# Performance work log

Hardware: AMD Instinct MI355X
Metric: run time of the kernel (lower is better)

The kernel has to match this reference:

```python
import jax, jax.numpy as jnp
import numpy as np

NUM_EXPERTS = 8
TOP_K = 2
N_EMBD = 1024
BLOCK_SIZE = 128
# d_ffn = round_up(4*n_embd // top_k, block_size)
D_FFN = ((4 * N_EMBD // TOP_K + BLOCK_SIZE - 1) // BLOCK_SIZE) * BLOCK_SIZE  # 2048
TOTAL_WIDTH = NUM_EXPERTS * D_FFN  # 16384


def setup_inputs() -> dict:
    key = jax.random.key(0)
    k1, k2, k3, k4 = jax.random.split(key, 4)
    x = jax.random.normal(k1, (4, 2048, N_EMBD), dtype=jnp.float32)
    # router: nn.Linear(n_embd, num_experts, bias=False) -> weight [E, n_embd]
    w_router = jax.random.normal(k2, (NUM_EXPERTS, N_EMBD), dtype=jnp.float32) * 0.02
    w1 = jax.random.normal(k3, (N_EMBD, TOTAL_WIDTH), dtype=jnp.float32) * 0.02
    w2 = jax.random.normal(k4, (TOTAL_WIDTH, N_EMBD), dtype=jnp.float32) * 0.02
    return {"x": x, "w_router": w_router, "w1": w1, "w2": w2}


def reference(x, w_router, w1, w2):
    B, S, N = x.shape
    T = B * S
    x_flat = x.reshape(T, N)

    # Router
    router_logits = x_flat @ w_router.T                       # [T, E]
    router_probs = jax.nn.softmax(router_logits.astype(jnp.float32), axis=-1)
    expert_weights, selected_experts = jax.lax.top_k(router_probs, TOP_K)  # [T, K]
    # norm_topk_prob=True
    expert_weights = expert_weights / expert_weights.sum(axis=-1, keepdims=True)
    expert_weights = expert_weights.astype(x.dtype)

    # Expert computation. The original does a sort/gather + block-sparse grouped
    # GEMM; math-equivalently, each token's output is
    #   sum_k w_k * gelu(x @ W1_e) @ W2_e  for e = selected_experts[:, k].
    # Loop over the small fixed expert set, masking per-token combine weights.
    out = jnp.zeros((T, N), dtype=x.dtype)
    for e in range(NUM_EXPERTS):
        off = e * D_FFN
        # combine weight for expert e per token (0 if not routed there)
        w_e = jnp.where(selected_experts == e, expert_weights, 0.0).sum(axis=-1)  # [T]
        h = jax.nn.gelu(x_flat @ w1[:, off:off + D_FFN], approximate=False)       # [T, D_FFN]
        out = out + w_e[:, None] * (h @ w2[off:off + D_FFN, :])

    output = out.reshape(B, S, N)

    # Aux losses
    router_z_loss = jnp.mean(jax.nn.logsumexp(router_logits, axis=-1) ** 2)
    p_i = router_probs.mean(axis=0).astype(x.dtype)            # [E]
    flat_sel = selected_experts.reshape(-1)
    f_i = jnp.zeros((NUM_EXPERTS,), dtype=x.dtype).at[flat_sel].add(1.0 / flat_sel.shape[0])
    load_balance_loss = NUM_EXPERTS * (f_i @ p_i)

    return output, router_z_loss, load_balance_loss, f_i
```

## Files before the change

### kernel.cpp

```cpp
#include <hip/hip_runtime.h>
#include <hip/hip_bf16.h>
#include <math.h>

#define T_TOK 8192
#define NE 1024
#define N_EXP 8
#define DFFN 2048
#define TW 16384
#define P_TOT 16384

#define BMT 128
#define BNT 128
#define BK9 32

typedef __attribute__((ext_vector_type(8))) short bf16x8;
typedef __attribute__((ext_vector_type(4))) float f32x4;

#define GLOAD_LDS16(g, l) __builtin_amdgcn_global_load_lds( \
    (const __attribute__((address_space(1))) void*)(g), \
    (__attribute__((address_space(3))) void*)(l), 16, 0, 0)

static __device__ __forceinline__ unsigned short f2bf(float f) {
    __hip_bfloat16 b = __float2bfloat16(f);
    return *(unsigned short*)&b;
}

static __device__ __forceinline__ float gelu_fast(float v) {
    float u2 = v * (1.5957691216f + 0.0713548162f * v * v);
    return v / (1.f + __expf(-u2));
}

__global__ __launch_bounds__(256) void router_kernel(
    const float* __restrict__ x, const float* __restrict__ wr,
    int* __restrict__ sel_idx, float* __restrict__ sel_wt,
    float* __restrict__ z_part, float* __restrict__ p_part,
    unsigned short* __restrict__ xb)
{
    __shared__ float wrs[N_EXP * NE];
    __shared__ float zred[32];
    __shared__ float pred[32][8];
    int tid = threadIdx.x;
    for (int i = tid; i < N_EXP * NE / 4; i += 256)
        ((float4*)wrs)[i] = ((const float4*)wr)[i];
    __syncthreads();

    int slot = tid >> 3, oct = tid & 7;
    int t = blockIdx.x * 32 + slot;
    float lg[N_EXP];
#pragma unroll
    for (int e = 0; e < N_EXP; e++) lg[e] = 0.f;

    const float4* x4 = (const float4*)(x + (size_t)t * NE) + oct * 32;
    for (int n4 = 0; n4 < 32; n4++) {
        float4 xv = x4[n4];
        ushort4 o;
        o.x = f2bf(xv.x); o.y = f2bf(xv.y); o.z = f2bf(xv.z); o.w = f2bf(xv.w);
        *(ushort4*)&xb[(size_t)t * NE + oct * 128 + n4 * 4] = o;
#pragma unroll
        for (int e = 0; e < N_EXP; e++) {
            const float* w = &wrs[e * NE + oct * 128 + n4 * 4];
            lg[e] += xv.x * w[0] + xv.y * w[1] + xv.z * w[2] + xv.w * w[3];
        }
    }
#pragma unroll
    for (int d = 1; d < 8; d <<= 1)
#pragma unroll
        for (int e = 0; e < N_EXP; e++) lg[e] += __shfl_xor(lg[e], d);

    float m = lg[0];
#pragma unroll
    for (int e = 1; e < N_EXP; e++) m = fmaxf(m, lg[e]);
    float p[N_EXP], s = 0.f;
#pragma unroll
    for (int e = 0; e < N_EXP; e++) { p[e] = expf(lg[e] - m); s += p[e]; }
    float inv = 1.f / s;
#pragma unroll
    for (int e = 0; e < N_EXP; e++) p[e] *= inv;
    float lse = m + logf(s);

    int e0 = 0;
#pragma unroll
    for (int e = 1; e < N_EXP; e++) if (p[e] > p[e0]) e0 = e;
    int e1 = (e0 == 0) ? 1 : 0;
#pragma unroll
    for (int e = 0; e < N_EXP; e++) if (e != e0 && p[e] > p[e1]) e1 = e;

    if (oct == 0) {
        float wn = 1.f / (p[e0] + p[e1]);
        sel_idx[t * 2 + 0] = e0;
        sel_idx[t * 2 + 1] = e1;
        sel_wt[t * 2 + 0] = p[e0] * wn;
        sel_wt[t * 2 + 1] = p[e1] * wn;
        zred[slot] = lse * lse;
#pragma unroll
        for (int e = 0; e < N_EXP; e++) pred[slot][e] = p[e];
    }
    __syncthreads();
    if (tid == 0) {
        float zs = 0.f;
        for (int i = 0; i < 32; i++) zs += zred[i];
        z_part[blockIdx.x] = zs;
        for (int e = 0; e < N_EXP; e++) {
            float ps = 0.f;
            for (int i = 0; i < 32; i++) ps += pred[i][e];
            p_part[blockIdx.x * N_EXP + e] = ps;
        }
    }
}

__global__ __launch_bounds__(256) void finalize_router(
    const int* __restrict__ sel_idx,
    const float* __restrict__ z_part, const float* __restrict__ p_part,
    int* __restrict__ cnt, int* __restrict__ off, int* __restrict__ cursor,
    int* __restrict__ tile_tab, int* __restrict__ tile_n,
    float* __restrict__ out)
{
    __shared__ int redc[256];
    __shared__ int cnts[N_EXP];
    int tid = threadIdx.x;
    int c[N_EXP];
#pragma unroll
    for (int e = 0; e < N_EXP; e++) c[e] = 0;
    for (int i = tid; i < P_TOT; i += 256) c[sel_idx[i]]++;
#pragma unroll
    for (int e = 0; e < N_EXP; e++) {
        redc[tid] = c[e];
        __syncthreads();
        for (int st = 128; st > 0; st >>= 1) {
            if (tid < st) redc[tid] += redc[tid + st];
            __syncthreads();
        }
        if (tid == 0) cnts[e] = redc[0];
        __syncthreads();
    }
    if (tid == 0) {
        int o = 0;
        int nt = 0;
        for (int e = 0; e < N_EXP; e++) {
            cnt[e] = cnts[e];
            off[e] = o;
            o += cnts[e];
            cursor[e] = 0;
            for (int rb = 0; rb < cnts[e]; rb += BMT)
                tile_tab[nt++] = (e << 20) | rb;
        }
        off[N_EXP] = o;
        tile_n[0] = nt;
        float zs = 0.f;
        for (int b = 0; b < 256; b++) zs += z_part[b];
        float lb = 0.f;
        float* tail = out + (size_t)T_TOK * NE;
        for (int e = 0; e < N_EXP; e++) {
            float ps = 0.f;
            for (int b = 0; b < 256; b++) ps += p_part[b * N_EXP + e];
            float fi = (float)cnts[e] / (float)P_TOT;
            float pi = ps / (float)T_TOK;
            lb += fi * pi;
            tail[2 + e] = fi;
        }
        tail[0] = zs / (float)T_TOK;
        tail[1] = 8.f * lb;
    }
}

__global__ __launch_bounds__(256) void scatter_kernel(
    const int* __restrict__ sel_idx, const int* __restrict__ off,
    int* __restrict__ cursor, int* __restrict__ token_list)
{
    int i = blockIdx.x * 256 + threadIdx.x;
    if (i < P_TOT) {
        int e = sel_idx[i];
        int pos = atomicAdd(&cursor[e], 1);
        token_list[off[e] + pos] = i;
    }
}

__global__ __launch_bounds__(256) void transpose_bf16_kernel(
    const float* __restrict__ src, unsigned short* __restrict__ dst,
    int R, int C)
{
    __shared__ float tile[64][65];
    int rb = blockIdx.y * 64, cb = blockIdx.x * 64;
    int tid = threadIdx.x;
#pragma unroll
    for (int p = 0; p < 4; p++) {
        int idx = p * 256 + tid;
        int r = idx >> 4, c4 = (idx & 15) << 2;
        float4 v = *(const float4*)&src[(size_t)(rb + r) * C + cb + c4];
        tile[r][c4 + 0] = v.x; tile[r][c4 + 1] = v.y;
        tile[r][c4 + 2] = v.z; tile[r][c4 + 3] = v.w;
    }
    __syncthreads();
#pragma unroll
    for (int p = 0; p < 4; p++) {
        int idx = p * 256 + tid;
        int c = idx >> 4, r4 = (idx & 15) << 2;
        ushort4 o;
        o.x = f2bf(tile[r4 + 0][c]); o.y = f2bf(tile[r4 + 1][c]);
        o.z = f2bf(tile[r4 + 2][c]); o.w = f2bf(tile[r4 + 3][c]);
        *(ushort4*)&dst[(size_t)(cb + c) * R + rb + r4] = o;
    }
}

#define STG(buf, kb) do {                                                 \
    GLOAD_LDS16(asrc0 + (kb), &As[buf][wid * 1024]);                      \
    GLOAD_LDS16(asrc1 + (kb), &As[buf][wid * 1024 + 512]);                \
    GLOAD_LDS16(bsrc0 + (kb), &Bs[buf][wid * 1024]);                      \
    GLOAD_LDS16(bsrc1 + (kb), &Bs[buf][wid * 1024 + 512]);                \
} while (0)

#define GEMM_LOOP(NKT)                                                    \
    STG(0, 0);                                                            \
    for (int t = 0; t < (NKT); t++) {                                     \
        int cur = t & 1;                                                  \
        if (t + 1 < (NKT)) {                                              \
            STG(cur ^ 1, (t + 1) * BK9);                                  \
            asm volatile("s_waitcnt vmcnt(4)" ::: "memory");              \
        } else {                                                          \
            asm volatile("s_waitcnt vmcnt(0)" ::: "memory");              \
        }                                                                 \
        __builtin_amdgcn_s_barrier();                                     \
        __builtin_amdgcn_sched_barrier(0);                                \
        bf16x8 af[4], bfr[4];                                             \
        _Pragma("unroll")                                                 \
        for (int m = 0; m < 4; m++)                                       \
            af[m] = *(const bf16x8*)&As[cur][(wm * 64 + m * 16 + rr) * BK9 + kqa * 8]; \
        _Pragma("unroll")                                                 \
        for (int n = 0; n < 4; n++)                                       \
            bfr[n] = *(const bf16x8*)&Bs[cur][(wn * 64 + n * 16 + rr) * BK9 + kqa * 8]; \
        __builtin_amdgcn_s_setprio(1);                                    \
        _Pragma("unroll")                                                 \
        for (int m = 0; m < 4; m++)                                       \
            _Pragma("unroll")                                             \
            for (int n = 0; n < 4; n++)                                   \
                acc[m][n] = __builtin_amdgcn_mfma_f32_16x16x32_bf16(      \
                    af[m], bfr[n], acc[m][n], 0, 0, 0);                   \
        __builtin_amdgcn_s_setprio(0);                                    \
        __builtin_amdgcn_sched_barrier(0);                                \
        __builtin_amdgcn_s_barrier();                                     \
    }

__global__ __launch_bounds__(256, 4) void gemm1_mfma(
    const __hip_bfloat16* __restrict__ xb, const __hip_bfloat16* __restrict__ w1t,
    const int* __restrict__ token_list, const float* __restrict__ sel_wt,
    const int* __restrict__ cnt, const int* __restrict__ off,
    const int* __restrict__ tile_tab, const int* __restrict__ tile_n,
    __hip_bfloat16* __restrict__ h)
{
    __shared__ __align__(16) __hip_bfloat16 As[2][BMT * BK9];
    __shared__ __align__(16) __hip_bfloat16 Bs[2][BNT * BK9];

    int b = blockIdx.x;
    int slot = b & 7, idx = b >> 3;
    int rowt = idx >> 1;
    if (rowt >= tile_n[0]) return;
    int colbase = (slot * 2 + (idx & 1)) * BNT;
    int tab = tile_tab[rowt];
    int e = tab >> 20, rowbase = tab & 0xFFFFF;
    int off_e = off[e];
    int rows_e = cnt[e] - rowbase;

    int tid = threadIdx.x;
    int wid = tid >> 6, lane = tid & 63;
    int wm = wid >> 1, wn = wid & 1;
    int rr = lane & 15, kq = lane >> 4;
    int kqa = kq ^ ((rr >> 1) & 3);
    int ksw = (lane & 3) ^ ((lane >> 3) & 3);

    int r0 = wid * 32 + (lane >> 2);
    int r1 = r0 + 16;
    int ent0 = token_list[off_e + rowbase + ((r0 < rows_e) ? r0 : 0)];
    int ent1 = token_list[off_e + rowbase + ((r1 < rows_e) ? r1 : 0)];
    const __hip_bfloat16* asrc0 = xb + (size_t)(ent0 >> 1) * NE + ksw * 8;
    const __hip_bfloat16* asrc1 = xb + (size_t)(ent1 >> 1) * NE + ksw * 8;
    const __hip_bfloat16* bsrc0 = w1t + (size_t)(e * DFFN + colbase + r0) * NE + ksw * 8;
    const __hip_bfloat16* bsrc1 = bsrc0 + (size_t)16 * NE;

    f32x4 acc[4][4] = {};
    GEMM_LOOP(NE / BK9)

    int colg = colbase + wn * 64;
#pragma unroll
    for (int m = 0; m < 4; m++) {
#pragma unroll
        for (int j = 0; j < 4; j++) {
            int r = wm * 64 + m * 16 + kq * 4 + j;
            if (r < rows_e) {
                size_t p = (size_t)off_e + rowbase + r;
                float wgt = sel_wt[token_list[p]];
#pragma unroll
                for (int n = 0; n < 4; n++) {
                    float g = gelu_fast(acc[m][n][j]);
                    h[p * DFFN + colg + n * 16 + rr] = __float2bfloat16(wgt * g);
                }
            }
        }
    }
}

__global__ __launch_bounds__(256, 4) void gemm2_mfma(
    const __hip_bfloat16* __restrict__ h, const __hip_bfloat16* __restrict__ w2t,
    const int* __restrict__ token_list,
    const int* __restrict__ cnt, const int* __restrict__ off,
    const int* __restrict__ tile_tab, const int* __restrict__ tile_n,
    float* __restrict__ out)
{
    __shared__ __align__(16) __hip_bfloat16 As[2][BMT * BK9];
    __shared__ __align__(16) __hip_bfloat16 Bs[2][BNT * BK9];

    int b = blockIdx.x;
    int slot = b & 7, rowt = b >> 3;
    if (rowt >= tile_n[0]) return;
    int colbase = slot * BNT;
    int tab = tile_tab[rowt];
    int e = tab >> 20, rowbase = tab & 0xFFFFF;
    int off_e = off[e];
    int rows_e = cnt[e] - rowbase;

    int tid = threadIdx.x;
    int wid = tid >> 6, lane = tid & 63;
    int wm = wid >> 1, wn = wid & 1;
    int rr = lane & 15, kq = lane >> 4;
    int kqa = kq ^ ((rr >> 1) & 3);
    int ksw = (lane & 3) ^ ((lane >> 3) & 3);

    int r0 = wid * 32 + (lane >> 2);
    int r1 = r0 + 16;
    int pr0 = off_e + rowbase + ((r0 < rows_e) ? r0 : 0);
    int pr1 = off_e + rowbase + ((r1 < rows_e) ? r1 : 0);
    const __hip_bfloat16* asrc0 = h + (size_t)pr0 * DFFN + ksw * 8;
    const __hip_bfloat16* asrc1 = h + (size_t)pr1 * DFFN + ksw * 8;
    const __hip_bfloat16* bsrc0 = w2t + (size_t)(colbase + r0) * TW + e * DFFN + ksw * 8;
    const __hip_bfloat16* bsrc1 = bsrc0 + (size_t)16 * TW;

    f32x4 acc[4][4] = {};
    GEMM_LOOP(DFFN / BK9)

    int colg = colbase + wn * 64;
#pragma unroll
    for (int m = 0; m < 4; m++) {
#pragma unroll
        for (int j = 0; j < 4; j++) {
            int r = wm * 64 + m * 16 + kq * 4 + j;
            if (r < rows_e) {
                size_t p = (size_t)off_e + rowbase + r;
                int tok = token_list[p] >> 1;
#pragma unroll
                for (int n = 0; n < 4; n++)
                    atomicAdd(&out[(size_t)tok * NE + colg + n * 16 + rr],
                              acc[m][n][j]);
            }
        }
    }
}

extern "C" void kernel_launch(void* const* d_in, const int* in_sizes, int n_in,
                              void* d_out, int out_size, void* d_ws, size_t ws_size,
                              hipStream_t stream)
{
    const float* x  = (const float*)d_in[0];
    const float* wr = (const float*)d_in[1];
    const float* w1 = (const float*)d_in[2];
    const float* w2 = (const float*)d_in[3];
    float* out = (float*)d_out;

    char* ws = (char*)d_ws;
    size_t o = 0;
    __hip_bfloat16* h   = (__hip_bfloat16*)(ws + o); o += (size_t)P_TOT * DFFN * 2;
    __hip_bfloat16* xb  = (__hip_bfloat16*)(ws + o); o += (size_t)T_TOK * NE * 2;
    __hip_bfloat16* w1t = (__hip_bfloat16*)(ws + o); o += (size_t)NE * TW * 2;
    __hip_bfloat16* w2t = (__hip_bfloat16*)(ws + o); o += (size_t)TW * NE * 2;
    int*   sel_idx    = (int*)(ws + o);   o += P_TOT * 4;
    float* sel_wt     = (float*)(ws + o); o += P_TOT * 4;
    int*   token_list = (int*)(ws + o);   o += P_TOT * 4;
    int*   cnt        = (int*)(ws + o);   o += 64;
    int*   off        = (int*)(ws + o);   o += 64;
    int*   cursor     = (int*)(ws + o);   o += 64;
    int*   tile_tab   = (int*)(ws + o);   o += 256 * 4;
    int*   tile_n     = (int*)(ws + o);   o += 64;
    float* z_part     = (float*)(ws + o); o += 256 * 4;
    float* p_part     = (float*)(ws + o); o += 256 * N_EXP * 4;

    hipMemsetAsync(d_out, 0, (size_t)out_size * sizeof(float), stream);

    router_kernel<<<256, 256, 0, stream>>>(x, wr, sel_idx, sel_wt, z_part, p_part,
                                           (unsigned short*)xb);
    transpose_bf16_kernel<<<dim3(TW / 64, NE / 64), 256, 0, stream>>>(
        w1, (unsigned short*)w1t, NE, TW);
    transpose_bf16_kernel<<<dim3(NE / 64, TW / 64), 256, 0, stream>>>(
        w2, (unsigned short*)w2t, TW, NE);
    finalize_router<<<1, 256, 0, stream>>>(sel_idx, z_part, p_part, cnt, off, cursor,
                                           tile_tab, tile_n, out);
    scatter_kernel<<<64, 256, 0, stream>>>(sel_idx, off, cursor, token_list);

    gemm1_mfma<<<2176, 256, 0, stream>>>(
        xb, w1t, token_list, sel_wt, cnt, off, tile_tab, tile_n, h);
    gemm2_mfma<<<1088, 256, 0, stream>>>(
        h, w2t, token_list, cnt, off, tile_tab, tile_n, out);
}
```

Measured before the change: 441.2 us.

## Use 256x256 tiles with 16 waves, 4-stage LDS ring, split-K GEMM2

Both expert GEMMs move from 128x128 tiles with 256 threads and double buffering to 256x256 tiles with 1024 threads (16 waves, each still computing a 64x64 sub-tile). The K-loop now uses a 4-deep LDS ring with a prefetch distance of two stages, which removes the trailing barrier in each iteration. GEMM2 also splits K into two halves across blocks and accumulates both halves with the existing atomics. The aim is more operand reuse per global load and fewer barriers; in exchange each block needs 128KB of dynamic LDS, fits only one block per CU, and GEMM2 doubles its atomic traffic.

```diff
diff --git a/kernel.cpp b/kernel.cpp
--- a/kernel.cpp
+++ b/kernel.cpp
@@ -9,9 +9,9 @@
 #define TW 16384
 #define P_TOT 16384
 
-#define BMT 128
-#define BNT 128
-#define BK9 32
+#define TILE_M 256
+#define TILE_N 256
+#define BKT 32
 
 typedef __attribute__((ext_vector_type(8))) short bf16x8;
 typedef __attribute__((ext_vector_type(4))) float f32x4;
@@ -141,7 +141,7 @@
             off[e] = o;
             o += cnts[e];
             cursor[e] = 0;
-            for (int rb = 0; rb < cnts[e]; rb += BMT)
+            for (int rb = 0; rb < cnts[e]; rb += TILE_M)
                 tile_tab[nt++] = (e << 20) | rb;
         }
         off[N_EXP] = o;
@@ -202,32 +202,32 @@
     }
 }
 
-#define STG(buf, kb) do {                                                 \
-    GLOAD_LDS16(asrc0 + (kb), &As[buf][wid * 1024]);                      \
-    GLOAD_LDS16(asrc1 + (kb), &As[buf][wid * 1024 + 512]);                \
-    GLOAD_LDS16(bsrc0 + (kb), &Bs[buf][wid * 1024]);                      \
-    GLOAD_LDS16(bsrc1 + (kb), &Bs[buf][wid * 1024 + 512]);                \
+#define STAGE11(buf, kb) do {                                             \
+    GLOAD_LDS16(asrc + (kb), Asm + (buf) * 8192 + wid * 512);             \
+    GLOAD_LDS16(bsrc + (kb), Bsm + (buf) * 8192 + wid * 512);             \
 } while (0)
 
-#define GEMM_LOOP(NKT)                                                    \
-    STG(0, 0);                                                            \
+#define GEMM_LOOP11(NKT)                                                  \
+    STAGE11(0, 0); STAGE11(1, BKT);                                       \
     for (int t = 0; t < (NKT); t++) {                                     \
-        int cur = t & 1;                                                  \
-        if (t + 1 < (NKT)) {                                              \
-            STG(cur ^ 1, (t + 1) * BK9);                                  \
+        if (t + 2 < (NKT)) {                                              \
+            STAGE11((t + 2) & 3, (t + 2) * BKT);                          \
             asm volatile("s_waitcnt vmcnt(4)" ::: "memory");              \
+        } else if (t + 1 < (NKT)) {                                       \
+            asm volatile("s_waitcnt vmcnt(2)" ::: "memory");              \
         } else {                                                          \
             asm volatile("s_waitcnt vmcnt(0)" ::: "memory");              \
         }                                                                 \
         __builtin_amdgcn_s_barrier();                                     \
         __builtin_amdgcn_sched_barrier(0);                                \
+        const int cur = t & 3;                                            \
         bf16x8 af[4], bfr[4];                                             \
         _Pragma("unroll")                                                 \
         for (int m = 0; m < 4; m++)                                       \
-            af[m] = *(const bf16x8*)&As[cur][(wm * 64 + m * 16 + rr) * BK9 + kqa * 8]; \
+            af[m] = *(const bf16x8*)&Asm[cur * 8192 + (wm * 64 + m * 16 + rr) * 32 + kqa * 8]; \
         _Pragma("unroll")                                                 \
         for (int n = 0; n < 4; n++)                                       \
-            bfr[n] = *(const bf16x8*)&Bs[cur][(wn * 64 + n * 16 + rr) * BK9 + kqa * 8]; \
+            bfr[n] = *(const bf16x8*)&Bsm[cur * 8192 + (wn * 64 + n * 16 + rr) * 32 + kqa * 8]; \
         __builtin_amdgcn_s_setprio(1);                                    \
         _Pragma("unroll")                                                 \
         for (int m = 0; m < 4; m++)                                       \
@@ -237,47 +237,45 @@
                     af[m], bfr[n], acc[m][n], 0, 0, 0);                   \
         __builtin_amdgcn_s_setprio(0);                                    \
         __builtin_amdgcn_sched_barrier(0);                                \
-        __builtin_amdgcn_s_barrier();                                     \
-    }
-
-__global__ __launch_bounds__(256, 4) void gemm1_mfma(
+    }
+
+#define GEMM_SETUP11()                                                    \
+    int tid = threadIdx.x;                                                \
+    int wid = tid >> 6, lane = tid & 63;                                  \
+    int wm = wid >> 2, wn = wid & 3;                                      \
+    int rr = lane & 15, kq = lane >> 4;                                   \
+    int kqa = kq ^ ((rr >> 1) & 3);                                       \
+    int ksw = (lane & 3) ^ ((lane >> 3) & 3);                             \
+    int arow = wid * 16 + (lane >> 2);
+
+__global__ __launch_bounds__(1024, 4) void gemm1_mfma(
     const __hip_bfloat16* __restrict__ xb, const __hip_bfloat16* __restrict__ w1t,
     const int* __restrict__ token_list, const float* __restrict__ sel_wt,
     const int* __restrict__ cnt, const int* __restrict__ off,
     const int* __restrict__ tile_tab, const int* __restrict__ tile_n,
     __hip_bfloat16* __restrict__ h)
 {
-    __shared__ __align__(16) __hip_bfloat16 As[2][BMT * BK9];
-    __shared__ __align__(16) __hip_bfloat16 Bs[2][BNT * BK9];
+    extern __shared__ __align__(16) __hip_bfloat16 smem[];
+    __hip_bfloat16* Asm = smem;
+    __hip_bfloat16* Bsm = smem + 32768;
 
     int b = blockIdx.x;
-    int slot = b & 7, idx = b >> 3;
-    int rowt = idx >> 1;
+    int slot = b & 7, rowt = b >> 3;
     if (rowt >= tile_n[0]) return;
-    int colbase = (slot * 2 + (idx & 1)) * BNT;
+    int colbase = slot * TILE_N;
     int tab = tile_tab[rowt];
     int e = tab >> 20, rowbase = tab & 0xFFFFF;
     int off_e = off[e];
     int rows_e = cnt[e] - rowbase;
 
-    int tid = threadIdx.x;
-    int wid = tid >> 6, lane = tid & 63;
-    int wm = wid >> 1, wn = wid & 1;
-    int rr = lane & 15, kq = lane >> 4;
-    int kqa = kq ^ ((rr >> 1) & 3);
-    int ksw = (lane & 3) ^ ((lane >> 3) & 3);
-
-    int r0 = wid * 32 + (lane >> 2);
-    int r1 = r0 + 16;
-    int ent0 = token_list[off_e + rowbase + ((r0 < rows_e) ? r0 : 0)];
-    int ent1 = token_list[off_e + rowbase + ((r1 < rows_e) ? r1 : 0)];
-    const __hip_bfloat16* asrc0 = xb + (size_t)(ent0 >> 1) * NE + ksw * 8;
-    const __hip_bfloat16* asrc1 = xb + (size_t)(ent1 >> 1) * NE + ksw * 8;
-    const __hip_bfloat16* bsrc0 = w1t + (size_t)(e * DFFN + colbase + r0) * NE + ksw * 8;
-    const __hip_bfloat16* bsrc1 = bsrc0 + (size_t)16 * NE;
+    GEMM_SETUP11()
+
+    int ent = token_list[off_e + rowbase + ((arow < rows_e) ? arow : 0)];
+    const __hip_bfloat16* asrc = xb + (size_t)(ent >> 1) * NE + ksw * 8;
+    const __hip_bfloat16* bsrc = w1t + (size_t)(e * DFFN + colbase + arow) * NE + ksw * 8;
 
     f32x4 acc[4][4] = {};
-    GEMM_LOOP(NE / BK9)
+    GEMM_LOOP11(NE / BKT)
 
     int colg = colbase + wn * 64;
 #pragma unroll
@@ -298,43 +296,35 @@
     }
 }
 
-__global__ __launch_bounds__(256, 4) void gemm2_mfma(
+__global__ __launch_bounds__(1024, 4) void gemm2_mfma(
     const __hip_bfloat16* __restrict__ h, const __hip_bfloat16* __restrict__ w2t,
     const int* __restrict__ token_list,
     const int* __restrict__ cnt, const int* __restrict__ off,
     const int* __restrict__ tile_tab, const int* __restrict__ tile_n,
     float* __restrict__ out)
 {
-    __shared__ __align__(16) __hip_bfloat16 As[2][BMT * BK9];
-    __shared__ __align__(16) __hip_bfloat16 Bs[2][BNT * BK9];
+    extern __shared__ __align__(16) __hip_bfloat16 smem[];
+    __hip_bfloat16* Asm = smem;
+    __hip_bfloat16* Bsm = smem + 32768;
 
     int b = blockIdx.x;
     int slot = b & 7, rowt = b >> 3;
     if (rowt >= tile_n[0]) return;
-    int colbase = slot * BNT;
+    int colbase = (slot >> 1) * TILE_N;
+    int k0 = (slot & 1) * (DFFN / 2);
     int tab = tile_tab[rowt];
     int e = tab >> 20, rowbase = tab & 0xFFFFF;
     int off_e = off[e];
     int rows_e = cnt[e] - rowbase;
 
-    int tid = threadIdx.x;
-    int wid = tid >> 6, lane = tid & 63;
-    int wm = wid >> 1, wn = wid & 1;
-    int rr = lane & 15, kq = lane >> 4;
-    int kqa = kq ^ ((rr >> 1) & 3);
-    int ksw = (lane & 3) ^ ((lane >> 3) & 3);
-
-    int r0 = wid * 32 + (lane >> 2);
-    int r1 = r0 + 16;
-    int pr0 = off_e + rowbase + ((r0 < rows_e) ? r0 : 0);
-    int pr1 = off_e + rowbase + ((r1 < rows_e) ? r1 : 0);
-    const __hip_bfloat16* asrc0 = h + (size_t)pr0 * DFFN + ksw * 8;
-    const __hip_bfloat16* asrc1 = h + (size_t)pr1 * DFFN + ksw * 8;
-    const __hip_bfloat16* bsrc0 = w2t + (size_t)(colbase + r0) * TW + e * DFFN + ksw * 8;
-    const __hip_bfloat16* bsrc1 = bsrc0 + (size_t)16 * TW;
+    GEMM_SETUP11()
+
+    int pr = off_e + rowbase + ((arow < rows_e) ? arow : 0);
+    const __hip_bfloat16* asrc = h + (size_t)pr * DFFN + k0 + ksw * 8;
+    const __hip_bfloat16* bsrc = w2t + (size_t)(colbase + arow) * TW + e * DFFN + k0 + ksw * 8;
 
     f32x4 acc[4][4] = {};
-    GEMM_LOOP(DFFN / BK9)
+    GEMM_LOOP11((DFFN / 2) / BKT)
 
     int colg = colbase + wn * 64;
 #pragma unroll
@@ -381,6 +371,11 @@
     float* z_part     = (float*)(ws + o); o += 256 * 4;
     float* p_part     = (float*)(ws + o); o += 256 * N_EXP * 4;
 
+    hipFuncSetAttribute((const void*)gemm1_mfma,
+                        hipFuncAttributeMaxDynamicSharedMemorySize, 131072);
+    hipFuncSetAttribute((const void*)gemm2_mfma,
+                        hipFuncAttributeMaxDynamicSharedMemorySize, 131072);
+
     hipMemsetAsync(d_out, 0, (size_t)out_size * sizeof(float), stream);
 
     router_kernel<<<256, 256, 0, stream>>>(x, wr, sel_idx, sel_wt, z_part, p_part,
@@ -393,8 +388,8 @@
                                            tile_tab, tile_n, out);
     scatter_kernel<<<64, 256, 0, stream>>>(sel_idx, off, cursor, token_list);
 
-    gemm1_mfma<<<2176, 256, 0, stream>>>(
+    gemm1_mfma<<<576, 1024, 131072, stream>>>(
         xb, w1t, token_list, sel_wt, cnt, off, tile_tab, tile_n, h);
-    gemm2_mfma<<<1088, 256, 0, stream>>>(
+    gemm2_mfma<<<576, 1024, 131072, stream>>>(
         h, w2t, token_list, cnt, off, tile_tab, tile_n, out);
 }
```

Result: slower. 461.4 us (+4.6%).

## Triple-buffer GEMM LDS pipeline, split-K gemm2, merge transpose launches

Applied to the files above, without the earlier changes.

Both grouped GEMMs move from double to triple LDS buffering. The prefetch for tile t+2 is issued after the current fragments are read, which removes the trailing barrier per k-step, and launch bounds are lowered to 3 blocks/CU to fit the larger LDS footprint. gemm2 is split in two along K with twice as many blocks, relying on the existing atomicAdd output to combine the halves, which doubles the atomic traffic. The two weight transposes are merged into one launch. Risks include reduced occupancy and a possible race, since the trailing barrier that protected buffer reuse is gone.

```diff
diff --git a/kernel.cpp b/kernel.cpp
--- a/kernel.cpp
+++ b/kernel.cpp
@@ -175,12 +175,23 @@
     }
 }
 
-__global__ __launch_bounds__(256) void transpose_bf16_kernel(
-    const float* __restrict__ src, unsigned short* __restrict__ dst,
-    int R, int C)
+__global__ __launch_bounds__(256) void transpose_both_kernel(
+    const float* __restrict__ w1, unsigned short* __restrict__ w1t,
+    const float* __restrict__ w2, unsigned short* __restrict__ w2t)
 {
     __shared__ float tile[64][65];
-    int rb = blockIdx.y * 64, cb = blockIdx.x * 64;
+    const float* src;
+    unsigned short* dst;
+    int R, C, rb, cb;
+    int bid = blockIdx.x;
+    if (bid < 4096) {
+        src = w1; dst = w1t; R = NE; C = TW;
+        cb = (bid & 255) * 64; rb = (bid >> 8) * 64;
+    } else {
+        int b2 = bid - 4096;
+        src = w2; dst = w2t; R = TW; C = NE;
+        cb = (b2 & 15) * 64; rb = (b2 >> 4) * 64;
+    }
     int tid = threadIdx.x;
 #pragma unroll
     for (int p = 0; p < 4; p++) {
@@ -203,18 +214,17 @@
 }
 
 #define STG(buf, kb) do {                                                 \
-    GLOAD_LDS16(asrc0 + (kb), &As[buf][wid * 1024]);                      \
-    GLOAD_LDS16(asrc1 + (kb), &As[buf][wid * 1024 + 512]);                \
-    GLOAD_LDS16(bsrc0 + (kb), &Bs[buf][wid * 1024]);                      \
-    GLOAD_LDS16(bsrc1 + (kb), &Bs[buf][wid * 1024 + 512]);                \
+    GLOAD_LDS16(asrc0 + (kb), &As[0][0] + (buf) * 4096 + wid * 1024);     \
+    GLOAD_LDS16(asrc1 + (kb), &As[0][0] + (buf) * 4096 + wid * 1024 + 512); \
+    GLOAD_LDS16(bsrc0 + (kb), &Bs[0][0] + (buf) * 4096 + wid * 1024);     \
+    GLOAD_LDS16(bsrc1 + (kb), &Bs[0][0] + (buf) * 4096 + wid * 1024 + 512); \
 } while (0)
 
 #define GEMM_LOOP(NKT)                                                    \
-    STG(0, 0);                                                            \
+    STG(0, 0); STG(1, BK9);                                               \
+    int cb0 = 0, cb1 = 1, cb2 = 2;                                        \
     for (int t = 0; t < (NKT); t++) {                                     \
-        int cur = t & 1;                                                  \
         if (t + 1 < (NKT)) {                                              \
-            STG(cur ^ 1, (t + 1) * BK9);                                  \
             asm volatile("s_waitcnt vmcnt(4)" ::: "memory");              \
         } else {                                                          \
             asm volatile("s_waitcnt vmcnt(0)" ::: "memory");              \
@@ -222,12 +232,15 @@
         __builtin_amdgcn_s_barrier();                                     \
         __builtin_amdgcn_sched_barrier(0);                                \
         bf16x8 af[4], bfr[4];                                             \
+        const __hip_bfloat16* Ac = &As[0][0] + cb0 * 4096;                \
+        const __hip_bfloat16* Bc = &Bs[0][0] + cb0 * 4096;                \
         _Pragma("unroll")                                                 \
         for (int m = 0; m < 4; m++)                                       \
-            af[m] = *(const bf16x8*)&As[cur][(wm * 64 + m * 16 + rr) * BK9 + kqa * 8]; \
+            af[m] = *(const bf16x8*)&Ac[(wm * 64 + m * 16 + rr) * BK9 + kqa * 8]; \
         _Pragma("unroll")                                                 \
         for (int n = 0; n < 4; n++)                                       \
-            bfr[n] = *(const bf16x8*)&Bs[cur][(wn * 64 + n * 16 + rr) * BK9 + kqa * 8]; \
+            bfr[n] = *(const bf16x8*)&Bc[(wn * 64 + n * 16 + rr) * BK9 + kqa * 8]; \
+        if (t + 2 < (NKT)) STG(cb2, (t + 2) * BK9);                       \
         __builtin_amdgcn_s_setprio(1);                                    \
         _Pragma("unroll")                                                 \
         for (int m = 0; m < 4; m++)                                       \
@@ -237,24 +250,24 @@
                     af[m], bfr[n], acc[m][n], 0, 0, 0);                   \
         __builtin_amdgcn_s_setprio(0);                                    \
         __builtin_amdgcn_sched_barrier(0);                                \
-        __builtin_amdgcn_s_barrier();                                     \
-    }
-
-__global__ __launch_bounds__(256, 4) void gemm1_mfma(
+        int cbt = cb0; cb0 = cb1; cb1 = cb2; cb2 = cbt;                   \
+    }
+
+__global__ __launch_bounds__(256, 3) void gemm1_mfma(
     const __hip_bfloat16* __restrict__ xb, const __hip_bfloat16* __restrict__ w1t,
     const int* __restrict__ token_list, const float* __restrict__ sel_wt,
     const int* __restrict__ cnt, const int* __restrict__ off,
     const int* __restrict__ tile_tab, const int* __restrict__ tile_n,
     __hip_bfloat16* __restrict__ h)
 {
-    __shared__ __align__(16) __hip_bfloat16 As[2][BMT * BK9];
-    __shared__ __align__(16) __hip_bfloat16 Bs[2][BNT * BK9];
+    __shared__ __align__(16) __hip_bfloat16 As[3][BMT * BK9];
+    __shared__ __align__(16) __hip_bfloat16 Bs[3][BNT * BK9];
 
     int b = blockIdx.x;
-    int slot = b & 7, idx = b >> 3;
-    int rowt = idx >> 1;
+    int slot = b & 7;
+    int rowt = b >> 4;
     if (rowt >= tile_n[0]) return;
-    int colbase = (slot * 2 + (idx & 1)) * BNT;
+    int colbase = (slot * 2 + ((b >> 3) & 1)) * BNT;
     int tab = tile_tab[rowt];
     int e = tab >> 20, rowbase = tab & 0xFFFFF;
     int off_e = off[e];
@@ -298,20 +311,22 @@
     }
 }
 
-__global__ __launch_bounds__(256, 4) void gemm2_mfma(
+__global__ __launch_bounds__(256, 3) void gemm2_mfma(
     const __hip_bfloat16* __restrict__ h, const __hip_bfloat16* __restrict__ w2t,
     const int* __restrict__ token_list,
     const int* __restrict__ cnt, const int* __restrict__ off,
     const int* __restrict__ tile_tab, const int* __restrict__ tile_n,
     float* __restrict__ out)
 {
-    __shared__ __align__(16) __hip_bfloat16 As[2][BMT * BK9];
-    __shared__ __align__(16) __hip_bfloat16 Bs[2][BNT * BK9];
+    __shared__ __align__(16) __hip_bfloat16 As[3][BMT * BK9];
+    __shared__ __align__(16) __hip_bfloat16 Bs[3][BNT * BK9];
 
     int b = blockIdx.x;
-    int slot = b & 7, rowt = b >> 3;
+    int slot = b & 7;
+    int rowt = b >> 4;
     if (rowt >= tile_n[0]) return;
     int colbase = slot * BNT;
+    int k0 = ((b >> 3) & 1) * (DFFN / 2);
     int tab = tile_tab[rowt];
     int e = tab >> 20, rowbase = tab & 0xFFFFF;
     int off_e = off[e];
@@ -328,13 +343,13 @@
     int r1 = r0 + 16;
     int pr0 = off_e + rowbase + ((r0 < rows_e) ? r0 : 0);
     int pr1 = off_e + rowbase + ((r1 < rows_e) ? r1 : 0);
-    const __hip_bfloat16* asrc0 = h + (size_t)pr0 * DFFN + ksw * 8;
-    const __hip_bfloat16* asrc1 = h + (size_t)pr1 * DFFN + ksw * 8;
-    const __hip_bfloat16* bsrc0 = w2t + (size_t)(colbase + r0) * TW + e * DFFN + ksw * 8;
+    const __hip_bfloat16* asrc0 = h + (size_t)pr0 * DFFN + k0 + ksw * 8;
+    const __hip_bfloat16* asrc1 = h + (size_t)pr1 * DFFN + k0 + ksw * 8;
+    const __hip_bfloat16* bsrc0 = w2t + (size_t)(colbase + r0) * TW + e * DFFN + k0 + ksw * 8;
     const __hip_bfloat16* bsrc1 = bsrc0 + (size_t)16 * TW;
 
     f32x4 acc[4][4] = {};
-    GEMM_LOOP(DFFN / BK9)
+    GEMM_LOOP((DFFN / 2) / BK9)
 
     int colg = colbase + wn * 64;
 #pragma unroll
@@ -385,16 +400,14 @@
 
     router_kernel<<<256, 256, 0, stream>>>(x, wr, sel_idx, sel_wt, z_part, p_part,
                                            (unsigned short*)xb);
-    transpose_bf16_kernel<<<dim3(TW / 64, NE / 64), 256, 0, stream>>>(
-        w1, (unsigned short*)w1t, NE, TW);
-    transpose_bf16_kernel<<<dim3(NE / 64, TW / 64), 256, 0, stream>>>(
-        w2, (unsigned short*)w2t, TW, NE);
+    transpose_both_kernel<<<8192, 256, 0, stream>>>(
+        w1, (unsigned short*)w1t, w2, (unsigned short*)w2t);
     finalize_router<<<1, 256, 0, stream>>>(sel_idx, z_part, p_part, cnt, off, cursor,
                                            tile_tab, tile_n, out);
     scatter_kernel<<<64, 256, 0, stream>>>(sel_idx, off, cursor, token_list);
 
     gemm1_mfma<<<2176, 256, 0, stream>>>(
         xb, w1t, token_list, sel_wt, cnt, off, tile_tab, tile_n, h);
-    gemm2_mfma<<<1088, 256, 0, stream>>>(
+    gemm2_mfma<<<2176, 256, 0, stream>>>(
         h, w2t, token_list, cnt, off, tile_tab, tile_n, out);
 }
```

Result: slower. 460.7 us (+4.4%).
